# Kernel tuning notes

Hardware: AMD Instinct MI355X
Metric: run time of the kernel (lower is better)

Reference implementation:

```python
import jax, jax.numpy as jnp
import numpy as np

H = 32          # hidden_size
IN = 32         # input_size
OUT = 1         # output_size
B, T = 4096, 168


def setup_inputs() -> dict:
    key = jax.random.key(0)
    ks = jax.random.split(key, 8)
    k = 1.0 / np.sqrt(H)  # torch nn.RNN init bound
    u = lambda kk, shape: jax.random.uniform(kk, shape, jnp.float32, -k, k)
    return {
        "x": jax.random.normal(ks[0], (B, T, IN), jnp.float32),
        "hidden": jax.random.normal(ks[1], (1, B, H), jnp.float32),
        "W_ih": u(ks[2], (H, IN)),
        "W_hh": u(ks[3], (H, H)),
        "b_ih": u(ks[4], (H,)),
        "b_hh": u(ks[5], (H,)),
        "W_out": u(ks[6], (OUT, H)),
        "b_out": u(ks[7], (OUT,)),
    }


def reference(x, hidden, W_ih, W_hh, b_ih, b_hh, W_out, b_out):
    # Elman RNN, relu nonlinearity, single layer, batch_first.
    # h_t = relu(x_t @ W_ih^T + b_ih + h_{t-1} @ W_hh^T + b_hh)
    h0 = hidden[0]                                   # [B, H]
    # Precompute the input projection for all timesteps in one big GEMM.
    xp = jnp.einsum('bti,hi->bth', x, W_ih) + (b_ih + b_hh)  # [B, T, H]
    xp_t = jnp.swapaxes(xp, 0, 1)                    # [T, B, H]

    def step(h, xt):
        h = jax.nn.relu(xt + h @ W_hh.T)
        return h, None

    hT, _ = jax.lax.scan(step, h0, xp_t)             # hT: [B, H] (last step)
    pred = hT @ W_out.T + b_out                      # [B, OUT]
    return pred, hT[None]                            # hidden: [1, B, H]
```

## Files before the change

kernel.cpp:

```cpp
#include <hip/hip_runtime.h>

#define HD 32
#define DP 8

typedef __attribute__((ext_vector_type(8))) short bf16x8;
typedef __attribute__((ext_vector_type(4))) float f32x4;

__device__ __forceinline__ int cvtpk_bf16(float a, float b) {
    int r;
    asm("v_cvt_pk_bf16_f32 %0, %1, %2" : "=v"(r) : "v"(a), "v"(b));
    return r;
}

__device__ __forceinline__ void split_pair(float a, float b, int& hi, int& lo) {
    hi = cvtpk_bf16(a, b);
    float fa = __int_as_float(hi << 16);
    float fb = __int_as_float((unsigned)hi & 0xffff0000u);
    lo = cvtpk_bf16(a - fa, b - fb);
}

__device__ __forceinline__ bf16x8 pack4(int w0, int w1, int w2, int w3) {
    union { int i[4]; bf16x8 v; } u;
    u.i[0] = w0; u.i[1] = w1; u.i[2] = w2; u.i[3] = w3;
    return u.v;
}

__device__ __forceinline__ void split_frag(f32x4 a, f32x4 b, bf16x8& hi, bf16x8& lo) {
    int h0,h1,h2,h3,l0,l1,l2,l3;
    split_pair(a[0], a[1], h0, l0);
    split_pair(a[2], a[3], h1, l1);
    split_pair(b[0], b[1], h2, l2);
    split_pair(b[2], b[3], h3, l3);
    hi = pack4(h0,h1,h2,h3);
    lo = pack4(l0,l1,l2,l3);
}

__device__ __forceinline__ bf16x8 to_bf16_frag(f32x4 a, f32x4 b) {
    return pack4(cvtpk_bf16(a[0], a[1]), cvtpk_bf16(a[2], a[3]),
                 cvtpk_bf16(b[0], b[1]), cvtpk_bf16(b[2], b[3]));
}

__device__ __forceinline__ void gload_pair(f32x4& a, f32x4& b, const float* sbase, int voff) {
    asm volatile("global_load_dwordx4 %0, %2, %3\n\t"
                 "global_load_dwordx4 %1, %2, %3 offset:16"
                 : "=&v"(a), "=&v"(b) : "v"(voff), "s"(sbase));
}

#define WAIT_TIE2(N, a, b) \
    asm volatile("s_waitcnt vmcnt(" #N ")" : "+v"(a), "+v"(b))
#define WAIT_TIE4(N, a, b, c, d) \
    asm volatile("s_waitcnt vmcnt(" #N ")" : "+v"(a), "+v"(b), "+v"(c), "+v"(d))

#define MFMA(a,b,c) __builtin_amdgcn_mfma_f32_16x16x32_bf16((a),(b),(c),0,0,0)

__global__ __launch_bounds__(64, 1)
void rnn_v6(const float* __restrict__ x,
            const float* __restrict__ h0p,
            const float* __restrict__ W_ih,
            const float* __restrict__ W_hh,
            const float* __restrict__ b_ih,
            const float* __restrict__ b_hh,
            const float* __restrict__ W_out,
            const float* __restrict__ b_out,
            float* __restrict__ out,
            int B, int T)
{
    const int l = threadIdx.x;
    const int q = l >> 4;
    const int c = l & 15;
    const int bglob = blockIdx.x * 16 + c;

    const int rA0 = ((c >> 2) << 3) + (c & 3);
    const int rA1 = rA0 + 4;

    bf16x8 Whh0h, Whh0l, Whh1h, Whh1l, Wih0h, Wih0l, Wih1h, Wih1l;
    {
        const f32x4* p;
        p = (const f32x4*)(W_hh + rA0 * HD + q * 8); split_frag(p[0], p[1], Whh0h, Whh0l);
        p = (const f32x4*)(W_hh + rA1 * HD + q * 8); split_frag(p[0], p[1], Whh1h, Whh1l);
        p = (const f32x4*)(W_ih + rA0 * HD + q * 8); split_frag(p[0], p[1], Wih0h, Wih0l);
        p = (const f32x4*)(W_ih + rA1 * HD + q * 8); split_frag(p[0], p[1], Wih1h, Wih1l);
    }

    f32x4 bias0, bias1;
#pragma unroll
    for (int r = 0; r < 4; ++r) {
        bias0[r] = b_ih[q*8 + r]     + b_hh[q*8 + r];
        bias1[r] = b_ih[q*8 + 4 + r] + b_hh[q*8 + 4 + r];
    }

    bf16x8 h_bf;
    {
        const f32x4* p = (const f32x4*)(h0p + (size_t)bglob * HD + q * 8);
        f32x4 a = p[0], b = p[1];
        h_bf = to_bf16_frag(a, b);
    }

    const int voff = (int)(((size_t)bglob * T * HD + q * 8) * 4);

    f32x4 xa[DP], xb[DP];
#pragma unroll
    for (int s = 0; s < DP; ++s)
        gload_pair(xa[s], xb[s], x + (size_t)s * HD, voff);

    f32x4 xpA0, xpA1, xpB0, xpB1;
    {
        WAIT_TIE2(14, xa[0], xb[0]);
        bf16x8 xbf = to_bf16_frag(xa[0], xb[0]);
        xpA0 = MFMA(Wih0h, xbf, bias0);
        xpA1 = MFMA(Wih1h, xbf, bias1);
        xpA0 = MFMA(Wih0l, xbf, xpA0);
        xpA1 = MFMA(Wih1l, xbf, xpA1);
    }
    {
        WAIT_TIE2(12, xa[1], xb[1]);
        bf16x8 xbf = to_bf16_frag(xa[1], xb[1]);
        xpB0 = MFMA(Wih0h, xbf, bias0);
        xpB1 = MFMA(Wih1h, xbf, bias1);
        xpB0 = MFMA(Wih0l, xbf, xpB0);
        xpB1 = MFMA(Wih1l, xbf, xpB1);
    }

    f32x4 hA = {0,0,0,0}, hB = {0,0,0,0};

    for (int t0 = 0; t0 < T; t0 += DP) {
#pragma unroll
        for (int s = 0; s < DP; s += 2) {
            const int t = t0 + s;
            f32x4 a0 = MFMA(Whh0h, h_bf, xpA0);
            f32x4 a1 = MFMA(Whh1h, h_bf, xpA1);
            a0 = MFMA(Whh0l, h_bf, a0);
            a1 = MFMA(Whh1l, h_bf, a1);

            int k1 = t + DP;     k1 = (k1 < T) ? k1 : (T - 1);
            int k2 = t + DP + 1; k2 = (k2 < T) ? k2 : (T - 1);
            gload_pair(xa[s],     xb[s],     x + (size_t)k1 * HD, voff);
            gload_pair(xa[s + 1], xb[s + 1], x + (size_t)k2 * HD, voff);

            const int s2 = (s + 2) & (DP - 1);
            const int s3 = (s + 3) & (DP - 1);
            WAIT_TIE4(12, xa[s2], xb[s2], xa[s3], xb[s3]);

            {
                bf16x8 xbf = to_bf16_frag(xa[s2], xb[s2]);
                xpA0 = MFMA(Wih0h, xbf, bias0);
                xpA1 = MFMA(Wih1h, xbf, bias1);
                xpA0 = MFMA(Wih0l, xbf, xpA0);
                xpA1 = MFMA(Wih1l, xbf, xpA1);
            }

#pragma unroll
            for (int r = 0; r < 4; ++r) {
                a0[r] = fmaxf(a0[r], 0.0f);
                a1[r] = fmaxf(a1[r], 0.0f);
            }
            h_bf = pack4(cvtpk_bf16(a0[0], a0[1]), cvtpk_bf16(a0[2], a0[3]),
                         cvtpk_bf16(a1[0], a1[1]), cvtpk_bf16(a1[2], a1[3]));

            f32x4 b0 = MFMA(Whh0h, h_bf, xpB0);
            f32x4 b1 = MFMA(Whh1h, h_bf, xpB1);
            b0 = MFMA(Whh0l, h_bf, b0);
            b1 = MFMA(Whh1l, h_bf, b1);

            {
                bf16x8 xbf = to_bf16_frag(xa[s3], xb[s3]);
                xpB0 = MFMA(Wih0h, xbf, bias0);
                xpB1 = MFMA(Wih1h, xbf, bias1);
                xpB0 = MFMA(Wih0l, xbf, xpB0);
                xpB1 = MFMA(Wih1l, xbf, xpB1);
            }

#pragma unroll
            for (int r = 0; r < 4; ++r) {
                b0[r] = fmaxf(b0[r], 0.0f);
                b1[r] = fmaxf(b1[r], 0.0f);
            }
            h_bf = pack4(cvtpk_bf16(b0[0], b0[1]), cvtpk_bf16(b0[2], b0[3]),
                         cvtpk_bf16(b1[0], b1[1]), cvtpk_bf16(b1[2], b1[3]));
            hA = b0; hB = b1;
        }
    }

    float* outh = out + B + (size_t)bglob * HD;
#pragma unroll
    for (int r = 0; r < 4; ++r) {
        outh[q*8 + r]     = hA[r];
        outh[q*8 + 4 + r] = hB[r];
    }
    float p = 0.0f;
#pragma unroll
    for (int r = 0; r < 4; ++r)
        p += hA[r] * W_out[q*8 + r] + hB[r] * W_out[q*8 + 4 + r];
    p += __shfl_xor(p, 16, 64);
    p += __shfl_xor(p, 32, 64);
    if (q == 0) out[bglob] = p + b_out[0];
}

extern "C" void kernel_launch(void* const* d_in, const int* in_sizes, int n_in,
                              void* d_out, int out_size, void* d_ws, size_t ws_size,
                              hipStream_t stream) {
    const float* x      = (const float*)d_in[0];
    const float* hidden = (const float*)d_in[1];
    const float* W_ih   = (const float*)d_in[2];
    const float* W_hh   = (const float*)d_in[3];
    const float* b_ih   = (const float*)d_in[4];
    const float* b_hh   = (const float*)d_in[5];
    const float* W_out  = (const float*)d_in[6];
    const float* b_out  = (const float*)d_in[7];
    float* out = (float*)d_out;

    const int B = in_sizes[1] / HD;
    const int T = in_sizes[0] / (B * HD);

    rnn_v6<<<dim3(B / 16), dim3(64), 0, stream>>>(
        x, hidden, W_ih, W_hh, b_ih, b_hh, W_out, b_out, out, B, T);
}
```

Before: 27.38 us.

## Use single bf16 W_ih, deepen x prefetch, and apply packed ReLU after conversion

The input projection now uses a single bf16 copy of W_ih instead of a hi/lo split. This halves the input-projection MFMAs that share the matrix pipe with the serial recurrence, at the cost of some precision in that projection. Separately, ReLU is applied to the packed bf16 hidden pairs with one v_pk_max_f16 per pair, replacing eight fp32 max instructions. This shortens the dependency chain between recurrent steps, though it relies on f16 comparison semantics matching bf16 for the sign test. The x prefetch ring is also deepened from 8 to 12 timesteps, with the vmcnt waits adjusted to match, and a final fp32 ReLU is added for the output state.

```diff
diff --git a/kernel.cpp b/kernel.cpp
--- a/kernel.cpp
+++ b/kernel.cpp
@@ -1,7 +1,7 @@
 #include <hip/hip_runtime.h>
 
 #define HD 32
-#define DP 8
+#define DP 12
 
 typedef __attribute__((ext_vector_type(8))) short bf16x8;
 typedef __attribute__((ext_vector_type(4))) float f32x4;
@@ -40,6 +40,12 @@
                  cvtpk_bf16(b[0], b[1]), cvtpk_bf16(b[2], b[3]));
 }
 
+__device__ __forceinline__ int pk_relu(int v) {
+    int r;
+    asm("v_pk_max_f16 %0, %1, 0" : "=v"(r) : "v"(v));
+    return r;
+}
+
 __device__ __forceinline__ void gload_pair(f32x4& a, f32x4& b, const float* sbase, int voff) {
     asm volatile("global_load_dwordx4 %0, %2, %3\n\t"
                  "global_load_dwordx4 %1, %2, %3 offset:16"
@@ -54,7 +60,7 @@
 #define MFMA(a,b,c) __builtin_amdgcn_mfma_f32_16x16x32_bf16((a),(b),(c),0,0,0)
 
 __global__ __launch_bounds__(64, 1)
-void rnn_v6(const float* __restrict__ x,
+void rnn_v7(const float* __restrict__ x,
             const float* __restrict__ h0p,
             const float* __restrict__ W_ih,
             const float* __restrict__ W_hh,
@@ -73,13 +79,13 @@
     const int rA0 = ((c >> 2) << 3) + (c & 3);
     const int rA1 = rA0 + 4;
 
-    bf16x8 Whh0h, Whh0l, Whh1h, Whh1l, Wih0h, Wih0l, Wih1h, Wih1l;
+    bf16x8 Whh0h, Whh0l, Whh1h, Whh1l, Wih0, Wih1;
     {
         const f32x4* p;
         p = (const f32x4*)(W_hh + rA0 * HD + q * 8); split_frag(p[0], p[1], Whh0h, Whh0l);
         p = (const f32x4*)(W_hh + rA1 * HD + q * 8); split_frag(p[0], p[1], Whh1h, Whh1l);
-        p = (const f32x4*)(W_ih + rA0 * HD + q * 8); split_frag(p[0], p[1], Wih0h, Wih0l);
-        p = (const f32x4*)(W_ih + rA1 * HD + q * 8); split_frag(p[0], p[1], Wih1h, Wih1l);
+        p = (const f32x4*)(W_ih + rA0 * HD + q * 8); Wih0 = to_bf16_frag(p[0], p[1]);
+        p = (const f32x4*)(W_ih + rA1 * HD + q * 8); Wih1 = to_bf16_frag(p[0], p[1]);
     }
 
     f32x4 bias0, bias1;
@@ -92,8 +98,7 @@
     bf16x8 h_bf;
     {
         const f32x4* p = (const f32x4*)(h0p + (size_t)bglob * HD + q * 8);
-        f32x4 a = p[0], b = p[1];
-        h_bf = to_bf16_frag(a, b);
+        h_bf = to_bf16_frag(p[0], p[1]);
     }
 
     const int voff = (int)(((size_t)bglob * T * HD + q * 8) * 4);
@@ -105,20 +110,16 @@
 
     f32x4 xpA0, xpA1, xpB0, xpB1;
     {
-        WAIT_TIE2(14, xa[0], xb[0]);
+        WAIT_TIE2(22, xa[0], xb[0]);
         bf16x8 xbf = to_bf16_frag(xa[0], xb[0]);
-        xpA0 = MFMA(Wih0h, xbf, bias0);
-        xpA1 = MFMA(Wih1h, xbf, bias1);
-        xpA0 = MFMA(Wih0l, xbf, xpA0);
-        xpA1 = MFMA(Wih1l, xbf, xpA1);
-    }
-    {
-        WAIT_TIE2(12, xa[1], xb[1]);
+        xpA0 = MFMA(Wih0, xbf, bias0);
+        xpA1 = MFMA(Wih1, xbf, bias1);
+    }
+    {
+        WAIT_TIE2(20, xa[1], xb[1]);
         bf16x8 xbf = to_bf16_frag(xa[1], xb[1]);
-        xpB0 = MFMA(Wih0h, xbf, bias0);
-        xpB1 = MFMA(Wih1h, xbf, bias1);
-        xpB0 = MFMA(Wih0l, xbf, xpB0);
-        xpB1 = MFMA(Wih1l, xbf, xpB1);
+        xpB0 = MFMA(Wih0, xbf, bias0);
+        xpB1 = MFMA(Wih1, xbf, bias1);
     }
 
     f32x4 hA = {0,0,0,0}, hB = {0,0,0,0};
@@ -137,25 +138,20 @@
             gload_pair(xa[s],     xb[s],     x + (size_t)k1 * HD, voff);
             gload_pair(xa[s + 1], xb[s + 1], x + (size_t)k2 * HD, voff);
 
-            const int s2 = (s + 2) & (DP - 1);
-            const int s3 = (s + 3) & (DP - 1);
-            WAIT_TIE4(12, xa[s2], xb[s2], xa[s3], xb[s3]);
+            const int s2 = (s + 2) % DP;
+            const int s3 = (s + 3) % DP;
+            WAIT_TIE4(20, xa[s2], xb[s2], xa[s3], xb[s3]);
 
             {
                 bf16x8 xbf = to_bf16_frag(xa[s2], xb[s2]);
-                xpA0 = MFMA(Wih0h, xbf, bias0);
-                xpA1 = MFMA(Wih1h, xbf, bias1);
-                xpA0 = MFMA(Wih0l, xbf, xpA0);
-                xpA1 = MFMA(Wih1l, xbf, xpA1);
+                xpA0 = MFMA(Wih0, xbf, bias0);
+                xpA1 = MFMA(Wih1, xbf, bias1);
             }
 
-#pragma unroll
-            for (int r = 0; r < 4; ++r) {
-                a0[r] = fmaxf(a0[r], 0.0f);
-                a1[r] = fmaxf(a1[r], 0.0f);
-            }
-            h_bf = pack4(cvtpk_bf16(a0[0], a0[1]), cvtpk_bf16(a0[2], a0[3]),
-                         cvtpk_bf16(a1[0], a1[1]), cvtpk_bf16(a1[2], a1[3]));
+            h_bf = pack4(pk_relu(cvtpk_bf16(a0[0], a0[1])),
+                         pk_relu(cvtpk_bf16(a0[2], a0[3])),
+                         pk_relu(cvtpk_bf16(a1[0], a1[1])),
+                         pk_relu(cvtpk_bf16(a1[2], a1[3])));
 
             f32x4 b0 = MFMA(Whh0h, h_bf, xpB0);
             f32x4 b1 = MFMA(Whh1h, h_bf, xpB1);
@@ -164,21 +160,22 @@
 
             {
                 bf16x8 xbf = to_bf16_frag(xa[s3], xb[s3]);
-                xpB0 = MFMA(Wih0h, xbf, bias0);
-                xpB1 = MFMA(Wih1h, xbf, bias1);
-                xpB0 = MFMA(Wih0l, xbf, xpB0);
-                xpB1 = MFMA(Wih1l, xbf, xpB1);
+                xpB0 = MFMA(Wih0, xbf, bias0);
+                xpB1 = MFMA(Wih1, xbf, bias1);
             }
 
-#pragma unroll
-            for (int r = 0; r < 4; ++r) {
-                b0[r] = fmaxf(b0[r], 0.0f);
-                b1[r] = fmaxf(b1[r], 0.0f);
-            }
-            h_bf = pack4(cvtpk_bf16(b0[0], b0[1]), cvtpk_bf16(b0[2], b0[3]),
-                         cvtpk_bf16(b1[0], b1[1]), cvtpk_bf16(b1[2], b1[3]));
+            h_bf = pack4(pk_relu(cvtpk_bf16(b0[0], b0[1])),
+                         pk_relu(cvtpk_bf16(b0[2], b0[3])),
+                         pk_relu(cvtpk_bf16(b1[0], b1[1])),
+                         pk_relu(cvtpk_bf16(b1[2], b1[3])));
             hA = b0; hB = b1;
         }
+    }
+
+#pragma unroll
+    for (int r = 0; r < 4; ++r) {
+        hA[r] = fmaxf(hA[r], 0.0f);
+        hB[r] = fmaxf(hB[r], 0.0f);
     }
 
     float* outh = out + B + (size_t)bglob * HD;
@@ -212,6 +209,6 @@
     const int B = in_sizes[1] / HD;
     const int T = in_sizes[0] / (B * HD);
 
-    rnn_v6<<<dim3(B / 16), dim3(64), 0, stream>>>(
+    rnn_v7<<<dim3(B / 16), dim3(64), 0, stream>>>(
         x, hidden, W_ih, W_hh, b_ih, b_hh, W_out, b_out, out, B, T);
 }
```

After: 23.42 us. 1.17x faster.
